# Kernel optimization log

Measured on AMD Instinct MI355X. Metric: run time of the kernel, lower is better.

## Reference

```python
import jax, jax.numpy as jnp
import numpy as np

DISCOUNT_FACTOR = 0.99
EPS = 1e-8


def setup_inputs() -> dict:
    key = jax.random.key(0)
    k1, k2, k3 = jax.random.split(key, 3)
    B, S = 8192, 1024
    # raw params initialized exactly like the torch module: atanh(target)
    raw_gamma = jnp.arctanh(jnp.array([DISCOUNT_FACTOR], dtype=jnp.float32))
    # create_init_lambda_sequence(0.5, S): linear ramp with mean == AVERAGE_LAMBDA
    lam_init = jnp.linspace(0.1, 0.9, S).astype(jnp.float32)
    raw_lambd = jnp.arctanh(lam_init)
    values = jax.random.normal(k1, (B, S + 1, 1), dtype=jnp.float32)
    rewards = jax.random.normal(k2, (B, S, 1), dtype=jnp.float32)
    dones = jax.random.randint(k3, (B, S, 1), 0, 2).astype(jnp.int32)
    return {
        "raw_gamma": raw_gamma,
        "raw_lambd": raw_lambd,
        "values": values,
        "rewards": rewards,
        "dones": dones,
        "input_seq_len": 1024,
    }


def reference(raw_gamma, raw_lambd, values, rewards, dones, input_seq_len):
    # gamma / lambd properties: tanh then clamp_min(1e-8)
    gamma = jnp.maximum(jnp.tanh(raw_gamma), EPS)[0]            # scalar
    lambd = jnp.maximum(jnp.tanh(raw_lambd), EPS)               # [max_seq_len]
    lam_seq = lambd[-input_seq_len:]                            # [S]

    # ---- update_sum_reward_weights (runs under no_grad in torch) ----
    # backward recurrence: v[t] = gamma * (1 - lam[t] + lam[t] * v[t+1]),  v[S] = 1
    def w_step(v_next, lam_t):
        v_t = gamma * (1.0 - lam_t + lam_t * v_next)
        return v_t, jnp.maximum(1.0 - v_t, EPS)

    _, w = jax.lax.scan(
        w_step,
        jnp.asarray(1.0, values.dtype),
        jax.lax.stop_gradient(lam_seq),
        reverse=True,
    )  # w: [S]
    srw = w / jnp.maximum(w.mean(), EPS)
    sum_reward_weights = jax.lax.stop_gradient(srw)[None, :, None]  # [1, S, 1]

    # ---- calculate_lambda_returns ----
    # ret[t] = r[t] + gamma*(1-done[t]) * ((1-lam[t])*V[t+1] + lam[t]*ret[t+1])
    d = dones.astype(values.dtype)
    v_next = values[:, 1:, :]                                   # [B, S, 1]
    xs = (
        jnp.swapaxes(rewards, 0, 1),   # [S, B, 1]
        jnp.swapaxes(d, 0, 1),         # [S, B, 1]
        jnp.swapaxes(v_next, 0, 1),    # [S, B, 1]
        lam_seq,                       # [S]
    )

    def r_step(ret_next, x):
        r, dn, vn, lam = x
        ret = r + gamma * (1.0 - dn) * ((1.0 - lam) * vn + lam * ret_next)
        return ret, ret

    _, rets = jax.lax.scan(r_step, values[:, -1, :], xs, reverse=True)  # [S, B, 1]
    lambda_returns = jnp.swapaxes(rets, 0, 1)                           # [B, S, 1]
    return lambda_returns, sum_reward_weights
```

## Files before the change

### kernel.cpp

```cpp
#include <hip/hip_runtime.h>
#include <math.h>

#define EPSF 1e-8f

typedef float nvec4 __attribute__((ext_vector_type(4)));
typedef int   nivec4 __attribute__((ext_vector_type(4)));

__device__ __forceinline__ float pick(nvec4 v, int i) {
    return i == 0 ? v.x : i == 1 ? v.y : i == 2 ? v.z : v.w;
}

__device__ __forceinline__ void suffix_scan64(float& A, float& B, int lane) {
#pragma unroll
    for (int d = 1; d < 64; d <<= 1) {
        float Ao = __shfl_down(A, d);
        float Bo = __shfl_down(B, d);
        if (lane + d < 64) {
            A = fmaf(B, Ao, A);
            B = B * Bo;
        }
    }
}

__global__ __launch_bounds__(256, 8)
void td_kernel(const float* __restrict__ raw_gamma,
               const float* __restrict__ raw_lambd, int lam_off,
               const float* __restrict__ values,
               const float* __restrict__ rewards,
               const int* __restrict__ dones,
               float* __restrict__ out, int B, int S)
{
    __shared__ float sA[4], sB[4];
    const int lane = threadIdx.x & 63;
    const int c    = threadIdx.x >> 6;
    const float gamma = fmaxf(tanhf(raw_gamma[0]), EPSF);

    if ((int)blockIdx.x == B) {
        if (threadIdx.x >= 64) return;
        const int base = lane << 4;
        float a[16], b[16];
#pragma unroll
        for (int k = 0; k < 4; ++k) {
            float4 l4 = *(const float4*)(raw_lambd + lam_off + base + 4 * k);
            float lv[4] = {l4.x, l4.y, l4.z, l4.w};
#pragma unroll
            for (int j = 0; j < 4; ++j) {
                float g1 = gamma * fmaxf(tanhf(lv[j]), EPSF);
                b[4 * k + j] = g1;
                a[4 * k + j] = gamma - g1;
            }
        }
        float A = a[15], Bc = b[15];
#pragma unroll
        for (int j = 14; j >= 0; --j) { A = fmaf(b[j], A, a[j]); Bc *= b[j]; }
        suffix_scan64(A, Bc, lane);
        float EA = __shfl_down(A, 1);
        float EB = __shfl_down(Bc, 1);
        if (lane == 63) { EA = 0.0f; EB = 1.0f; }
        float v = EA + EB;
        float w[16], sum = 0.0f;
#pragma unroll
        for (int j = 15; j >= 0; --j) {
            v = fmaf(b[j], v, a[j]);
            w[j] = fmaxf(1.0f - v, EPSF);
            sum += w[j];
        }
#pragma unroll
        for (int d = 32; d; d >>= 1) sum += __shfl_xor(sum, d);
        float inv = 1.0f / fmaxf(sum / (float)S, EPSF);
        float* srw = out + (size_t)B * S;
#pragma unroll
        for (int j = 0; j < 16; ++j) srw[base + j] = w[j] * inv;
        return;
    }

    const int r  = blockIdx.x;
    const int C  = S >> 2;
    const int t0 = c * C + (lane << 2);
    const size_t rb = (size_t)r * (S + 1);

    nvec4  r4 = __builtin_nontemporal_load((const nvec4*)(rewards + (size_t)r * S + t0));
    nivec4 d4 = __builtin_nontemporal_load((const nivec4*)(dones + (size_t)r * S + t0));

    const int sh = (r + 1) & 3;
    const size_t E  = rb + (size_t)c * C + 1;
    const size_t A0 = E - sh;
    nvec4 m4 = __builtin_nontemporal_load((const nvec4*)(values + A0) + lane);
    size_t A0t = A0 + 256;
    const size_t last4 = (size_t)B * (S + 1) - 4;
    if (A0t > last4) A0t = last4;
    nvec4 t4 = __builtin_nontemporal_load((const nvec4*)(values + A0t));
    const int delta = (int)(A0 + 256 - A0t);
    float vS = values[rb + S];

    float4 l4 = *(const float4*)(raw_lambd + lam_off + t0);
    float lv[4] = {l4.x, l4.y, l4.z, l4.w};
    float g1v[4];
#pragma unroll
    for (int j = 0; j < 4; ++j)
        g1v[j] = gamma * fmaxf(tanhf(lv[j]), EPSF);

    float n0 = __shfl_down(m4.x, 1);
    float n1 = __shfl_down(m4.y, 1);
    float n2 = __shfl_down(m4.z, 1);
    if (lane == 63) {
        n0 = pick(t4, delta);
        n1 = pick(t4, delta + 1 > 3 ? 3 : delta + 1);
        n2 = pick(t4, delta + 2 > 3 ? 3 : delta + 2);
    }
    float vn0, vn1, vn2, vn3;
    if (sh == 0)      { vn0 = m4.x; vn1 = m4.y; vn2 = m4.z; vn3 = m4.w; }
    else if (sh == 1) { vn0 = m4.y; vn1 = m4.z; vn2 = m4.w; vn3 = n0; }
    else if (sh == 2) { vn0 = m4.z; vn1 = m4.w; vn2 = n0;   vn3 = n1; }
    else              { vn0 = m4.w; vn1 = n0;   vn2 = n1;   vn3 = n2; }

    float vn[4] = {vn0, vn1, vn2, vn3};
    float rr[4] = {r4.x, r4.y, r4.z, r4.w};
    int   di[4] = {d4.x, d4.y, d4.z, d4.w};
    float a[4], b[4];
#pragma unroll
    for (int j = 0; j < 4; ++j) {
        float ndn = 1.0f - (float)di[j];
        b[j] = g1v[j] * ndn;
        a[j] = fmaf((gamma - g1v[j]) * vn[j], ndn, rr[j]);
    }

    float A = a[3], Bc = b[3];
#pragma unroll
    for (int j = 2; j >= 0; --j) { A = fmaf(b[j], A, a[j]); Bc *= b[j]; }
    suffix_scan64(A, Bc, lane);
    float EA = __shfl_down(A, 1);
    float EB = __shfl_down(Bc, 1);
    if (lane == 63) { EA = 0.0f; EB = 1.0f; }
    if (lane == 0) { sA[c] = A; sB[c] = Bc; }
    __syncthreads();

    float x = vS;
#pragma unroll
    for (int j = 3; j >= 1; --j)
        if (j > c) x = fmaf(sB[j], x, sA[j]);

    float xi = fmaf(EB, x, EA);
    float o3 = fmaf(b[3], xi, a[3]);
    float o2 = fmaf(b[2], o3, a[2]);
    float o1 = fmaf(b[1], o2, a[1]);
    float o0 = fmaf(b[0], o1, a[0]);
    nvec4 ov = {o0, o1, o2, o3};
    __builtin_nontemporal_store(ov, (nvec4*)(out + (size_t)r * S + t0));
}

extern "C" void kernel_launch(void* const* d_in, const int* in_sizes, int n_in,
                              void* d_out, int out_size, void* d_ws, size_t ws_size,
                              hipStream_t stream) {
    const float* raw_gamma = (const float*)d_in[0];
    const float* raw_lambd = (const float*)d_in[1];
    const float* values    = (const float*)d_in[2];
    const float* rewards   = (const float*)d_in[3];
    const int*   dones     = (const int*)d_in[4];
    float* out = (float*)d_out;

    int n_v = in_sizes[2];
    int n_r = in_sizes[3];
    int B = n_v - n_r;
    int S = n_r / B;
    int lam_off = in_sizes[1] - S;

    td_kernel<<<B + 1, 256, 0, stream>>>(
        raw_gamma, raw_lambd, lam_off, values, rewards, dones, out, B, S);
}
```

Baseline: 138.1 us.

## Process four rows per block with software-prefetched next-row loads

Each block now handles four consecutive batch rows instead of one. While the current row's scan runs, the rewards, dones and values for the next row are loaded, and shared-memory partials are double-buffered so only one barrier is needed per row. The lambda tanh setup is hoisted so it runs once per block rather than once per row. This cuts the block count by four and relaxes the launch bound so more registers can hold the prefetched data, at the cost of less block-level parallelism and a serial row loop inside each block.

```diff
diff --git a/kernel.cpp b/kernel.cpp
--- a/kernel.cpp
+++ b/kernel.cpp
@@ -22,20 +22,20 @@
     }
 }
 
-__global__ __launch_bounds__(256, 8)
+__global__ __launch_bounds__(256, 4)
 void td_kernel(const float* __restrict__ raw_gamma,
                const float* __restrict__ raw_lambd, int lam_off,
                const float* __restrict__ values,
                const float* __restrict__ rewards,
                const int* __restrict__ dones,
-               float* __restrict__ out, int B, int S)
+               float* __restrict__ out, int B, int S, int nBlocks)
 {
-    __shared__ float sA[4], sB[4];
+    __shared__ float sA[2][4], sB[2][4];
     const int lane = threadIdx.x & 63;
     const int c    = threadIdx.x >> 6;
     const float gamma = fmaxf(tanhf(raw_gamma[0]), EPSF);
 
-    if ((int)blockIdx.x == B) {
+    if ((int)blockIdx.x == nBlocks) {
         if (threadIdx.x >= 64) return;
         const int base = lane << 4;
         float a[16], b[16];
@@ -74,79 +74,102 @@
         return;
     }
 
-    const int r  = blockIdx.x;
+    const int r0 = blockIdx.x * 4;
     const int C  = S >> 2;
     const int t0 = c * C + (lane << 2);
-    const size_t rb = (size_t)r * (S + 1);
-
-    nvec4  r4 = __builtin_nontemporal_load((const nvec4*)(rewards + (size_t)r * S + t0));
-    nivec4 d4 = __builtin_nontemporal_load((const nivec4*)(dones + (size_t)r * S + t0));
-
-    const int sh = (r + 1) & 3;
-    const size_t E  = rb + (size_t)c * C + 1;
-    const size_t A0 = E - sh;
-    nvec4 m4 = __builtin_nontemporal_load((const nvec4*)(values + A0) + lane);
-    size_t A0t = A0 + 256;
     const size_t last4 = (size_t)B * (S + 1) - 4;
-    if (A0t > last4) A0t = last4;
-    nvec4 t4 = __builtin_nontemporal_load((const nvec4*)(values + A0t));
-    const int delta = (int)(A0 + 256 - A0t);
-    float vS = values[rb + S];
 
     float4 l4 = *(const float4*)(raw_lambd + lam_off + t0);
     float lv[4] = {l4.x, l4.y, l4.z, l4.w};
-    float g1v[4];
-#pragma unroll
-    for (int j = 0; j < 4; ++j)
-        g1v[j] = gamma * fmaxf(tanhf(lv[j]), EPSF);
-
-    float n0 = __shfl_down(m4.x, 1);
-    float n1 = __shfl_down(m4.y, 1);
-    float n2 = __shfl_down(m4.z, 1);
-    if (lane == 63) {
-        n0 = pick(t4, delta);
-        n1 = pick(t4, delta + 1 > 3 ? 3 : delta + 1);
-        n2 = pick(t4, delta + 2 > 3 ? 3 : delta + 2);
-    }
-    float vn0, vn1, vn2, vn3;
-    if (sh == 0)      { vn0 = m4.x; vn1 = m4.y; vn2 = m4.z; vn3 = m4.w; }
-    else if (sh == 1) { vn0 = m4.y; vn1 = m4.z; vn2 = m4.w; vn3 = n0; }
-    else if (sh == 2) { vn0 = m4.z; vn1 = m4.w; vn2 = n0;   vn3 = n1; }
-    else              { vn0 = m4.w; vn1 = n0;   vn2 = n1;   vn3 = n2; }
-
-    float vn[4] = {vn0, vn1, vn2, vn3};
-    float rr[4] = {r4.x, r4.y, r4.z, r4.w};
-    int   di[4] = {d4.x, d4.y, d4.z, d4.w};
-    float a[4], b[4];
+    float g1v[4], g0v[4];
 #pragma unroll
     for (int j = 0; j < 4; ++j) {
-        float ndn = 1.0f - (float)di[j];
-        b[j] = g1v[j] * ndn;
-        a[j] = fmaf((gamma - g1v[j]) * vn[j], ndn, rr[j]);
+        g1v[j] = gamma * fmaxf(tanhf(lv[j]), EPSF);
+        g0v[j] = gamma - g1v[j];
     }
 
-    float A = a[3], Bc = b[3];
+    nvec4 cr; nivec4 cd; nvec4 cm, ct; float cvS;
+    {
+        const size_t rb = (size_t)r0 * (S + 1);
+        cr = __builtin_nontemporal_load((const nvec4*)(rewards + (size_t)r0 * S + t0));
+        cd = __builtin_nontemporal_load((const nivec4*)(dones + (size_t)r0 * S + t0));
+        const int sh = (r0 + 1) & 3;
+        const size_t A0 = rb + (size_t)c * C + 1 - sh;
+        cm = __builtin_nontemporal_load((const nvec4*)(values + A0) + lane);
+        size_t A0t = A0 + 256;
+        if (A0t > last4) A0t = last4;
+        ct = __builtin_nontemporal_load((const nvec4*)(values + A0t));
+        cvS = values[rb + S];
+    }
+
+    int p = 0;
+#pragma unroll 1
+    for (int rr = 0; rr < 4; ++rr) {
+        const int r = r0 + rr;
+        const int sh = (r + 1) & 3;
+
+        nvec4 nr, nm, nt; nivec4 ndn4; float nvS = 0.0f;
+        if (rr < 3) {
+            const int rn = r + 1;
+            const size_t rbn = (size_t)rn * (S + 1);
+            nr = __builtin_nontemporal_load((const nvec4*)(rewards + (size_t)rn * S + t0));
+            ndn4 = __builtin_nontemporal_load((const nivec4*)(dones + (size_t)rn * S + t0));
+            const int shn = (rn + 1) & 3;
+            const size_t A0n = rbn + (size_t)c * C + 1 - shn;
+            nm = __builtin_nontemporal_load((const nvec4*)(values + A0n) + lane);
+            size_t A0tn = A0n + 256;
+            if (A0tn > last4) A0tn = last4;
+            nt = __builtin_nontemporal_load((const nvec4*)(values + A0tn));
+            nvS = values[rbn + S];
+        }
+
+        float n0 = __shfl_down(cm.x, 1);
+        float n1 = __shfl_down(cm.y, 1);
+        float n2 = __shfl_down(cm.z, 1);
+        if (lane == 63) { n0 = ct.x; n1 = ct.y; n2 = ct.z; }
+        float vn0, vn1, vn2, vn3;
+        if (sh == 0)      { vn0 = cm.x; vn1 = cm.y; vn2 = cm.z; vn3 = cm.w; }
+        else if (sh == 1) { vn0 = cm.y; vn1 = cm.z; vn2 = cm.w; vn3 = n0; }
+        else if (sh == 2) { vn0 = cm.z; vn1 = cm.w; vn2 = n0;   vn3 = n1; }
+        else              { vn0 = cm.w; vn1 = n0;   vn2 = n1;   vn3 = n2; }
+
+        float vn[4] = {vn0, vn1, vn2, vn3};
+        float rw[4] = {cr.x, cr.y, cr.z, cr.w};
+        int   di[4] = {cd.x, cd.y, cd.z, cd.w};
+        float a[4], b[4];
 #pragma unroll
-    for (int j = 2; j >= 0; --j) { A = fmaf(b[j], A, a[j]); Bc *= b[j]; }
-    suffix_scan64(A, Bc, lane);
-    float EA = __shfl_down(A, 1);
-    float EB = __shfl_down(Bc, 1);
-    if (lane == 63) { EA = 0.0f; EB = 1.0f; }
-    if (lane == 0) { sA[c] = A; sB[c] = Bc; }
-    __syncthreads();
+        for (int j = 0; j < 4; ++j) {
+            float ndd = 1.0f - (float)di[j];
+            b[j] = g1v[j] * ndd;
+            a[j] = fmaf(g0v[j] * vn[j], ndd, rw[j]);
+        }
 
-    float x = vS;
+        float A = a[3], Bc = b[3];
 #pragma unroll
-    for (int j = 3; j >= 1; --j)
-        if (j > c) x = fmaf(sB[j], x, sA[j]);
+        for (int j = 2; j >= 0; --j) { A = fmaf(b[j], A, a[j]); Bc *= b[j]; }
+        suffix_scan64(A, Bc, lane);
+        float EA = __shfl_down(A, 1);
+        float EB = __shfl_down(Bc, 1);
+        if (lane == 63) { EA = 0.0f; EB = 1.0f; }
+        if (lane == 0) { sA[p][c] = A; sB[p][c] = Bc; }
+        __syncthreads();
 
-    float xi = fmaf(EB, x, EA);
-    float o3 = fmaf(b[3], xi, a[3]);
-    float o2 = fmaf(b[2], o3, a[2]);
-    float o1 = fmaf(b[1], o2, a[1]);
-    float o0 = fmaf(b[0], o1, a[0]);
-    nvec4 ov = {o0, o1, o2, o3};
-    __builtin_nontemporal_store(ov, (nvec4*)(out + (size_t)r * S + t0));
+        float x = cvS;
+#pragma unroll
+        for (int j = 3; j >= 1; --j)
+            if (j > c) x = fmaf(sB[p][j], x, sA[p][j]);
+
+        float xi = fmaf(EB, x, EA);
+        float o3 = fmaf(b[3], xi, a[3]);
+        float o2 = fmaf(b[2], o3, a[2]);
+        float o1 = fmaf(b[1], o2, a[1]);
+        float o0 = fmaf(b[0], o1, a[0]);
+        nvec4 ov = {o0, o1, o2, o3};
+        __builtin_nontemporal_store(ov, (nvec4*)(out + (size_t)r * S + t0));
+
+        if (rr < 3) { cr = nr; cd = ndn4; cm = nm; ct = nt; cvS = nvS; }
+        p ^= 1;
+    }
 }
 
 extern "C" void kernel_launch(void* const* d_in, const int* in_sizes, int n_in,
@@ -165,6 +188,7 @@
     int S = n_r / B;
     int lam_off = in_sizes[1] - S;
 
-    td_kernel<<<B + 1, 256, 0, stream>>>(
-        raw_gamma, raw_lambd, lam_off, values, rewards, dones, out, B, S);
+    int nBlocks = B / 4;
+    td_kernel<<<nBlocks + 1, 256, 0, stream>>>(
+        raw_gamma, raw_lambd, lam_off, values, rewards, dones, out, B, S, nBlocks);
 }
```

New measurement: 141.7 us. 1.03x slower.
